# Optimization experiments

Hardware: AMD Instinct MI355X
Metric: run time of the kernel (lower is better)

Reference implementation:

```python
import jax, jax.numpy as jnp
import numpy as np

# Dims: batch, queries, graph nodes, text len, hidden, heads, layers, ffn
B, NQ, NN, T, D, H, LAYERS, FF = 16, 32, 128, 352, 768, 8, 6, 3072
L = NQ + NN + T          # 512 total sequence length
HD = D // H              # 96 head dim
NEG = -1e9               # additive mask value (HF uses dtype min; -1e9 is equivalent post-softmax)
LN_EPS = 1e-12           # BERT LayerNorm eps


def _ln(x, g, b):
    m = x.mean(-1, keepdims=True)
    v = ((x - m) ** 2).mean(-1, keepdims=True)
    return (x - m) * jax.lax.rsqrt(v + LN_EPS) * g + b


def setup_inputs() -> dict:
    key = jax.random.key(0)
    ks = iter(jax.random.split(key, 32))

    def nrm(shape, s=0.02):
        return jax.random.normal(next(ks), shape, jnp.float32) * s

    return {
        "graph_node_features": jax.random.normal(next(ks), (B, NN, D), jnp.float32),
        "text_embeds": jax.random.normal(next(ks), (B, T, D), jnp.float32),
        "text_atts": jnp.ones((B, T), jnp.int32),
        "graph_mask": jnp.ones((B, NN), jnp.int32),
        "query_tokens": nrm((1, NQ, D), 1.0),   # nn.Parameter(torch.randn(...))
        "gproj_w": nrm((D, D)), "gproj_b": jnp.zeros((D,)),
        "pos_emb": nrm((L, D)), "tok_emb": nrm((D,)),  # token_type row 0
        "emb_ln_g": jnp.ones((D,)), "emb_ln_b": jnp.zeros((D,)),
        "qkv_w": nrm((LAYERS, D, 3 * D)), "qkv_b": jnp.zeros((LAYERS, 3 * D)),
        "ao_w": nrm((LAYERS, D, D)), "ao_b": jnp.zeros((LAYERS, D)),
        "ln1_g": jnp.ones((LAYERS, D)), "ln1_b": jnp.zeros((LAYERS, D)),
        "ff1_w": nrm((LAYERS, D, FF)), "ff1_b": jnp.zeros((LAYERS, FF)),
        "ff2_w": nrm((LAYERS, FF, D)), "ff2_b": jnp.zeros((LAYERS, D)),
        "ln2_g": jnp.ones((LAYERS, D)), "ln2_b": jnp.zeros((LAYERS, D)),
    }


def _itg_bias(text_atts, graph_mask):
    # Build the custom ITG prefix-LM mask: bidirectional over [queries|graph],
    # causal over text, and queries/graph blocked from attending to text.
    keep = jnp.concatenate(
        [jnp.ones((B, NQ), jnp.int32), graph_mask, text_atts], axis=1)  # [B, L]
    ts = NQ + NN
    idx = jnp.arange(L)
    is_text = idx >= ts
    pair = (keep[:, :, None] * keep[:, None, :]).astype(bool)          # padding mask
    causal_ok = jnp.where(is_text[:, None] & is_text[None, :],
                          idx[:, None] >= idx[None, :], True)           # tril in text block
    block_ok = ~((~is_text)[:, None] & is_text[None, :])                # prefix cannot see text
    mask = pair & causal_ok & block_ok                                  # [B, L, L]
    return jnp.where(mask, 0.0, NEG)[:, None, :, :]                     # [B, 1, L, L]


def reference(graph_node_features, text_embeds, text_atts, graph_mask,
              query_tokens, gproj_w, gproj_b, pos_emb, tok_emb,
              emb_ln_g, emb_ln_b, qkv_w, qkv_b, ao_w, ao_b,
              ln1_g, ln1_b, ff1_w, ff1_b, ff2_w, ff2_b, ln2_g, ln2_b):
    gfeat = graph_node_features @ gproj_w + gproj_b
    qtok = jnp.broadcast_to(query_tokens, (B, NQ, D))
    x = jnp.concatenate([qtok, gfeat, text_embeds], axis=1)             # [B, L, D]
    bias = _itg_bias(text_atts, graph_mask)

    # BERT embeddings (inputs_embeds path): + position + token_type(0), LN (dropout off)
    x = _ln(x + pos_emb[None] + tok_emb, emb_ln_g, emb_ln_b)

    scale = 1.0 / np.sqrt(HD)
    for i in range(LAYERS):
        qkv = x @ qkv_w[i] + qkv_b[i]
        q, k, v = jnp.split(qkv, 3, axis=-1)
        q = q.reshape(B, L, H, HD)
        k = k.reshape(B, L, H, HD)
        v = v.reshape(B, L, H, HD)
        s = jnp.einsum('bqhd,bkhd->bhqk', q, k) * scale + bias
        p = jax.nn.softmax(s, axis=-1)
        ctx = jnp.einsum('bhqk,bkhd->bqhd', p, v).reshape(B, L, D)
        x = _ln(x + ctx @ ao_w[i] + ao_b[i], ln1_g[i], ln1_b[i])
        h = jax.nn.gelu(x @ ff1_w[i] + ff1_b[i], approximate=False)
        x = _ln(x + h @ ff2_w[i] + ff2_b[i], ln2_g[i], ln2_b[i])

    return x[:, NQ + NN:, :]   # text_feats [B, T, D]
```

## Files before the change

kernel.cpp:

```cpp
#include <hip/hip_runtime.h>
#include <math.h>

typedef __bf16 bf16;
typedef __bf16 bf16x8 __attribute__((ext_vector_type(8)));
typedef float f32x4 __attribute__((ext_vector_type(4)));

#define NQ   32
#define NN_  128
#define TT   352
#define DD   768
#define NH   8
#define HDIM 96
#define LSEQ 512
#define TSPLIT 160
#define FFD  3072
#define NLAYER 6
#define NBATCH 16

#define GLOAD(srcp, dstp)                                                     \
    __builtin_amdgcn_global_load_lds(                                         \
        (const __attribute__((address_space(1))) void*)(srcp),                \
        (__attribute__((address_space(3))) void*)(dstp), 16, 0, 0)

template <int ACT>
__global__ __launch_bounds__(256) void gemm_bt(
    const bf16* __restrict__ A, const bf16* __restrict__ Bt,
    bf16* __restrict__ C, const float* __restrict__ bias,
    int K, int lda, int ldb, int ldc, float alpha, int Nstore, size_t zstride)
{
    __shared__ __attribute__((aligned(16))) bf16 As[3 * 4096];
    __shared__ __attribute__((aligned(16))) bf16 Bs[3 * 4096];

    const int z = blockIdx.z;
    A  += (size_t)z * K;
    Bt += (size_t)z * K;
    C  += (size_t)z * zstride;

    const int n0 = blockIdx.x * 128, m0 = blockIdx.y * 128;
    const int t = threadIdx.x;
    const int w = t >> 6, l = t & 63;
    const int wm = w >> 1, wn = w & 1;
    const int lr = l & 15, quad = l >> 4;

    f32x4 acc[4][4] = {};

    const int f0 = w * 1024 + l * 8;
    const int ra0 = f0 >> 5, ca0 = f0 & 31;
    const int ra1 = (f0 + 512) >> 5, ca1 = (f0 + 512) & 31;
    const bf16* a0 = A  + (size_t)(m0 + ra0) * lda + ca0;
    const bf16* a1 = A  + (size_t)(m0 + ra1) * lda + ca1;
    const bf16* b0 = Bt + (size_t)(n0 + ra0) * ldb + ca0;
    const bf16* b1 = Bt + (size_t)(n0 + ra1) * ldb + ca1;

    const int nt = K >> 5;

    {
        bf16* pA = &As[w * 1024];
        bf16* pB = &Bs[w * 1024];
        GLOAD(a0, pA);        GLOAD(a1, pA + 512);
        GLOAD(b0, pB);        GLOAD(b1, pB + 512);
        pA += 4096;  pB += 4096;
        GLOAD(a0 + 32, pA);   GLOAD(a1 + 32, pA + 512);
        GLOAD(b0 + 32, pB);   GLOAD(b1 + 32, pB + 512);
    }

    int cb = 0, wb = 2;
    for (int T = 0; T < nt; ++T) {
        if (T == nt - 1) {
            asm volatile("s_waitcnt vmcnt(0)" ::: "memory");
        } else {
            asm volatile("s_waitcnt vmcnt(4)" ::: "memory");
        }
        __builtin_amdgcn_s_barrier();
        __builtin_amdgcn_sched_barrier(0);

        if (T + 2 < nt) {
            const int k0 = (T + 2) << 5;
            bf16* pA = &As[wb * 4096 + w * 1024];
            bf16* pB = &Bs[wb * 4096 + w * 1024];
            GLOAD(a0 + k0, pA);   GLOAD(a1 + k0, pA + 512);
            GLOAD(b0 + k0, pB);   GLOAD(b1 + k0, pB + 512);
        }

        const int cur = cb << 12;
        bf16x8 af[4], bf_[4];
#pragma unroll
        for (int i = 0; i < 4; ++i)
            af[i] = *(const bf16x8*)&As[cur + (wm * 64 + i * 16 + lr) * 32 + quad * 8];
#pragma unroll
        for (int j = 0; j < 4; ++j)
            bf_[j] = *(const bf16x8*)&Bs[cur + (wn * 64 + j * 16 + lr) * 32 + quad * 8];
#pragma unroll
        for (int i = 0; i < 4; ++i)
#pragma unroll
            for (int j = 0; j < 4; ++j)
                acc[i][j] = __builtin_amdgcn_mfma_f32_16x16x32_bf16(af[i], bf_[j], acc[i][j], 0, 0, 0);

        cb = (cb == 2) ? 0 : cb + 1;
        wb = (wb == 2) ? 0 : wb + 1;
    }

    const bool dob = (z == 0);
#pragma unroll
    for (int i = 0; i < 4; ++i) {
        const int grow = m0 + wm * 64 + i * 16 + quad * 4;
#pragma unroll
        for (int j = 0; j < 4; ++j) {
            const int gcol = n0 + wn * 64 + j * 16 + lr;
            if (gcol >= Nstore) continue;
            float bv = (bias && dob) ? bias[gcol] : 0.0f;
#pragma unroll
            for (int r = 0; r < 4; ++r) {
                float v = acc[i][j][r] * alpha + bv;
                if (ACT == 1) v = 0.5f * v * (1.0f + erff(v * 0.70710678118654752f));
                C[(size_t)(grow + r) * ldc + gcol] = (bf16)v;
            }
        }
    }
}

template <int ACT>
__global__ __launch_bounds__(512) void gemm_bt8(
    const bf16* __restrict__ A, const bf16* __restrict__ Bt,
    bf16* __restrict__ C, const float* __restrict__ bias,
    int K, int lda, int ldb, int ldc, float alpha, int Nstore)
{
    __shared__ __attribute__((aligned(16))) bf16 As[3 * 8192];
    __shared__ __attribute__((aligned(16))) bf16 Bs[3 * 4096];

    const int n0 = blockIdx.x * 128, m0 = blockIdx.y * 256;
    const int t = threadIdx.x;
    const int w = t >> 6, l = t & 63;
    const int wm = w >> 1, wn = w & 1;
    const int lr = l & 15, quad = l >> 4;

    f32x4 acc[4][4] = {};

    const int f0 = w * 512 + l * 8;
    const int ra0 = f0 >> 5,          ca0 = f0 & 31;
    const int ra1 = ((f0 + 4096) >> 5), ca1 = f0 & 31;
    const bf16* a0 = A  + (size_t)(m0 + ra0) * lda + ca0;
    const bf16* a1 = A  + (size_t)(m0 + ra1) * lda + ca1;
    const bf16* b0 = Bt + (size_t)(n0 + ra0) * ldb + ca0;

    const int nt = K >> 5;

    {
        bf16* pA = &As[w * 512];
        bf16* pB = &Bs[w * 512];
        GLOAD(a0, pA);        GLOAD(a1, pA + 4096);   GLOAD(b0, pB);
        pA += 8192;  pB += 4096;
        GLOAD(a0 + 32, pA);   GLOAD(a1 + 32, pA + 4096);  GLOAD(b0 + 32, pB);
    }

    int cb = 0, wb = 2;
    for (int T = 0; T < nt; ++T) {
        if (T == nt - 1) {
            asm volatile("s_waitcnt vmcnt(0)" ::: "memory");
        } else {
            asm volatile("s_waitcnt vmcnt(3)" ::: "memory");
        }
        __builtin_amdgcn_s_barrier();
        __builtin_amdgcn_sched_barrier(0);

        if (T + 2 < nt) {
            const int k0 = (T + 2) << 5;
            bf16* pA = &As[wb * 8192 + w * 512];
            bf16* pB = &Bs[wb * 4096 + w * 512];
            GLOAD(a0 + k0, pA);  GLOAD(a1 + k0, pA + 4096);  GLOAD(b0 + k0, pB);
        }

        const int curA = cb * 8192, curB = cb * 4096;
        bf16x8 af[4], bf_[4];
#pragma unroll
        for (int i = 0; i < 4; ++i)
            af[i] = *(const bf16x8*)&As[curA + (wm * 64 + i * 16 + lr) * 32 + quad * 8];
#pragma unroll
        for (int j = 0; j < 4; ++j)
            bf_[j] = *(const bf16x8*)&Bs[curB + (wn * 64 + j * 16 + lr) * 32 + quad * 8];

        __builtin_amdgcn_s_setprio(1);
#pragma unroll
        for (int i = 0; i < 4; ++i)
#pragma unroll
            for (int j = 0; j < 4; ++j)
                acc[i][j] = __builtin_amdgcn_mfma_f32_16x16x32_bf16(af[i], bf_[j], acc[i][j], 0, 0, 0);
        __builtin_amdgcn_s_setprio(0);

        cb = (cb == 2) ? 0 : cb + 1;
        wb = (wb == 2) ? 0 : wb + 1;
    }

#pragma unroll
    for (int i = 0; i < 4; ++i) {
        const int grow = m0 + wm * 64 + i * 16 + quad * 4;
#pragma unroll
        for (int j = 0; j < 4; ++j) {
            const int gcol = n0 + wn * 64 + j * 16 + lr;
            if (gcol >= Nstore) continue;
            float bv = bias ? bias[gcol] : 0.0f;
#pragma unroll
            for (int r = 0; r < 4; ++r) {
                float v = acc[i][j][r] * alpha + bv;
                if (ACT == 1) v = 0.5f * v * (1.0f + erff(v * 0.70710678118654752f));
                C[(size_t)(grow + r) * ldc + gcol] = (bf16)v;
            }
        }
    }
}

__global__ __launch_bounds__(256) void flash_attn(
    const bf16* __restrict__ qkv, bf16* __restrict__ ctx,
    const int* __restrict__ tatts, const int* __restrict__ gmask)
{
    __shared__ __attribute__((aligned(16))) bf16 Qs[64 * 104];
    __shared__ __attribute__((aligned(16))) bf16 Ks[64 * 104];
    __shared__ __attribute__((aligned(16))) bf16 Vs[96 * 72];
    __shared__ __attribute__((aligned(16))) bf16 Ps[64 * 72];
    __shared__ int keep[512];

    const int qt = blockIdx.x;
    const int bh = blockIdx.y;
    const int b = bh >> 3, h = bh & 7;
    const int q0 = qt * 64;
    const int t = threadIdx.x;
    const int w = t >> 6, l = t & 63;
    const int lr = l & 15, quad = l >> 4;
    const float scale = 0.10206207261596577f;

    const bf16* qbase = qkv + (size_t)b * 512 * 2304 + h * 96;
    const bf16* kbase = qbase + 768;
    const bf16* vbase = qbase + 1536;

    for (int j = t; j < 512; j += 256)
        keep[j] = (j < NQ) ? 1 : (j < TSPLIT ? gmask[b * NN_ + j - NQ]
                                             : tatts[b * TT + j - TSPLIT]);

#pragma unroll
    for (int c = 0; c < 3; ++c) {
        const int idx = t * 8 + c * 2048;
        const int r = idx / 96, d = idx % 96;
        *(bf16x8*)&Qs[r * 104 + d] =
            *(const bf16x8*)&qbase[(size_t)(q0 + r) * 2304 + d];
    }
    __syncthreads();

    int ki[4];
    int ig[4];
#pragma unroll
    for (int r = 0; r < 4; ++r) {
        ig[r] = q0 + w * 16 + quad * 4 + r;
        ki[r] = keep[ig[r]];
    }

    float m_run[4] = {-1e30f, -1e30f, -1e30f, -1e30f};
    float l_run[4] = {0.f, 0.f, 0.f, 0.f};
    f32x4 oc[6] = {};

    const int JMAX = (qt < 3) ? 128 : q0;
    for (int j0 = 0; j0 <= JMAX; j0 += 64) {
        __syncthreads();
#pragma unroll
        for (int c = 0; c < 3; ++c) {
            const int idx = t * 8 + c * 2048;
            const int r = idx / 96, d = idx % 96;
            *(bf16x8*)&Ks[r * 104 + d] =
                *(const bf16x8*)&kbase[(size_t)(j0 + r) * 2304 + d];
            bf16x8 vv = *(const bf16x8*)&vbase[(size_t)(j0 + r) * 2304 + d];
#pragma unroll
            for (int jj = 0; jj < 8; ++jj)
                Vs[(d + jj) * 72 + r] = vv[jj];
        }
        __syncthreads();

        bf16x8 aq[3];
#pragma unroll
        for (int ds = 0; ds < 3; ++ds)
            aq[ds] = *(const bf16x8*)&Qs[(w * 16 + lr) * 104 + ds * 32 + quad * 8];
        f32x4 sc[4];
#pragma unroll
        for (int cb = 0; cb < 4; ++cb) {
            f32x4 a = {};
#pragma unroll
            for (int ds = 0; ds < 3; ++ds) {
                bf16x8 bk = *(const bf16x8*)&Ks[(cb * 16 + lr) * 104 + ds * 32 + quad * 8];
                a = __builtin_amdgcn_mfma_f32_16x16x32_bf16(aq[ds], bk, a, 0, 0, 0);
            }
            sc[cb] = a;
        }

        float tm[4] = {-1e30f, -1e30f, -1e30f, -1e30f};
#pragma unroll
        for (int cb = 0; cb < 4; ++cb) {
            const int jg = j0 + cb * 16 + lr;
            const int kj = keep[jg];
#pragma unroll
            for (int r = 0; r < 4; ++r) {
                const int i = ig[r];
                bool ok = ki[r] && kj;
                if (i < TSPLIT && jg >= TSPLIT) ok = false;
                if (i >= TSPLIT && jg >= TSPLIT && i < jg) ok = false;
                float s = sc[cb][r] * scale + (ok ? 0.f : -1e9f);
                sc[cb][r] = s;
                tm[r] = fmaxf(tm[r], s);
            }
        }
#pragma unroll
        for (int off = 1; off < 16; off <<= 1)
#pragma unroll
            for (int r = 0; r < 4; ++r)
                tm[r] = fmaxf(tm[r], __shfl_xor(tm[r], off));

        float alpha_[4], ts[4] = {0.f, 0.f, 0.f, 0.f};
#pragma unroll
        for (int r = 0; r < 4; ++r) {
            const float mn = fmaxf(m_run[r], tm[r]);
            alpha_[r] = __expf(m_run[r] - mn);
            m_run[r] = mn;
            l_run[r] *= alpha_[r];
        }
#pragma unroll
        for (int db = 0; db < 6; ++db)
#pragma unroll
            for (int r = 0; r < 4; ++r)
                oc[db][r] *= alpha_[r];

#pragma unroll
        for (int cb = 0; cb < 4; ++cb)
#pragma unroll
            for (int r = 0; r < 4; ++r) {
                const float p = __expf(sc[cb][r] - m_run[r]);
                ts[r] += p;
                Ps[(w * 16 + quad * 4 + r) * 72 + cb * 16 + lr] = (bf16)p;
            }
#pragma unroll
        for (int off = 1; off < 16; off <<= 1)
#pragma unroll
            for (int r = 0; r < 4; ++r)
                ts[r] += __shfl_xor(ts[r], off);
#pragma unroll
        for (int r = 0; r < 4; ++r) l_run[r] += ts[r];

        __syncthreads();

#pragma unroll
        for (int l0 = 0; l0 < 64; l0 += 32) {
            bf16x8 ap = *(const bf16x8*)&Ps[(w * 16 + lr) * 72 + l0 + quad * 8];
#pragma unroll
            for (int db = 0; db < 6; ++db) {
                bf16x8 bv = *(const bf16x8*)&Vs[(db * 16 + lr) * 72 + l0 + quad * 8];
                oc[db] = __builtin_amdgcn_mfma_f32_16x16x32_bf16(ap, bv, oc[db], 0, 0, 0);
            }
        }
    }

#pragma unroll
    for (int r = 0; r < 4; ++r) {
        const float inv = 1.f / l_run[r];
        bf16* orow = ctx + ((size_t)b * 512 + ig[r]) * 768 + h * 96;
#pragma unroll
        for (int db = 0; db < 6; ++db)
            orow[db * 16 + lr] = (bf16)(oc[db][r] * inv);
    }
}

__global__ void transpose_w(const float* __restrict__ in, bf16* __restrict__ out,
                            int R, int C)
{
    __shared__ bf16 tile[32][33];
    const int c0 = blockIdx.x * 32, r0 = blockIdx.y * 32;
    const int tx = threadIdx.x & 31, ty = threadIdx.x >> 5;
    for (int i = ty; i < 32; i += 8)
        tile[i][tx] = (bf16)in[(size_t)(r0 + i) * C + c0 + tx];
    __syncthreads();
    for (int i = ty; i < 32; i += 8)
        out[(size_t)(c0 + i) * R + r0 + tx] = tile[tx][i];
}

__global__ void cvt_bf16(const float* __restrict__ in, bf16* __restrict__ out, int n)
{
    const int idx = blockIdx.x * 256 + threadIdx.x;
    if (idx < n) out[idx] = (bf16)in[idx];
}

__device__ __forceinline__ void block_reduce_2(float& a, float& b)
{
#pragma unroll
    for (int off = 32; off; off >>= 1) {
        a += __shfl_xor(a, off);
        b += __shfl_xor(b, off);
    }
    __shared__ float sa[4], sb[4];
    const int w = threadIdx.x >> 6;
    if ((threadIdx.x & 63) == 0) { sa[w] = a; sb[w] = b; }
    __syncthreads();
    a = sa[0] + sa[1] + sa[2] + sa[3];
    b = sb[0] + sb[1] + sb[2] + sb[3];
}

__global__ void embed_ln(const float* __restrict__ qtok, const bf16* __restrict__ gfeat,
                         const float* __restrict__ text, const float* __restrict__ pos,
                         const float* __restrict__ tok, const float* __restrict__ g,
                         const float* __restrict__ bb, bf16* __restrict__ x)
{
    const int row = blockIdx.x;
    const int l = row & 511, b = row >> 9;
    const int t = threadIdx.x;

    float vals[3], s = 0.f, sq = 0.f;
#pragma unroll
    for (int c = 0; c < 3; ++c) {
        const int d = t + c * 256;
        float base;
        if (l < NQ)           base = qtok[(size_t)l * DD + d];
        else if (l < TSPLIT)  base = (float)gfeat[((size_t)b * NN_ + (l - NQ)) * DD + d];
        else                  base = text[((size_t)b * TT + (l - TSPLIT)) * DD + d];
        float v = base + pos[(size_t)l * DD + d] + tok[d];
        vals[c] = v; s += v; sq += v * v;
    }
    block_reduce_2(s, sq);
    const float mean = s * (1.f / 768.f);
    const float var = sq * (1.f / 768.f) - mean * mean;
    const float rs = rsqrtf(var + 1e-12f);
    bf16* o = x + (size_t)row * DD;
#pragma unroll
    for (int c = 0; c < 3; ++c) {
        const int d = t + c * 256;
        o[d] = (bf16)((vals[c] - mean) * rs * g[d] + bb[d]);
    }
}

__global__ void ln_rows3(const bf16* __restrict__ X, const bf16* __restrict__ Y,
                         const bf16* __restrict__ Z, bf16* __restrict__ Out,
                         const float* __restrict__ g, const float* __restrict__ bb)
{
    const int row = blockIdx.x;
    const int t = threadIdx.x;
    const bf16* xr = X + (size_t)row * DD;
    const bf16* yr = Y + (size_t)row * DD;
    const bf16* zr = Z + (size_t)row * DD;
    float vals[3], s = 0.f, sq = 0.f;
#pragma unroll
    for (int c = 0; c < 3; ++c) {
        const int d = t + c * 256;
        float v = (float)xr[d] + (float)yr[d] + (float)zr[d];
        vals[c] = v; s += v; sq += v * v;
    }
    block_reduce_2(s, sq);
    const float mean = s * (1.f / 768.f);
    const float var = sq * (1.f / 768.f) - mean * mean;
    const float rs = rsqrtf(var + 1e-12f);
    bf16* o = Out + (size_t)row * DD;
#pragma unroll
    for (int c = 0; c < 3; ++c) {
        const int d = t + c * 256;
        o[d] = (bf16)((vals[c] - mean) * rs * g[d] + bb[d]);
    }
}

__global__ void copy_out(const bf16* __restrict__ x, float* __restrict__ out)
{
    const size_t idx = (size_t)blockIdx.x * 256 + threadIdx.x;
    const int d = idx % DD;
    const size_t row = idx / DD;
    const int t = row % TT;
    const int b = row / TT;
    out[idx] = (float)x[((size_t)b * LSEQ + TSPLIT + t) * DD + d];
}

static void launch_gemm(const bf16* A, const bf16* Bt, bf16* C, const float* bias,
                        int M, int K, int lda, int ldb, int ldc,
                        float alpha, int Nstore, int act, int ksplit, size_t zstride,
                        hipStream_t stream)
{
    dim3 grid((Nstore + 127) / 128, M / 128, ksplit);
    if (act)
        gemm_bt<1><<<grid, 256, 0, stream>>>(A, Bt, C, bias, K / ksplit, lda, ldb, ldc, alpha, Nstore, zstride);
    else
        gemm_bt<0><<<grid, 256, 0, stream>>>(A, Bt, C, bias, K / ksplit, lda, ldb, ldc, alpha, Nstore, zstride);
}

static void launch_gemm8(const bf16* A, const bf16* Bt, bf16* C, const float* bias,
                         int M, int K, int lda, int ldb, int ldc,
                         float alpha, int Nstore, int act, hipStream_t stream)
{
    dim3 grid((Nstore + 127) / 128, M / 256, 1);
    if (act)
        gemm_bt8<1><<<grid, 512, 0, stream>>>(A, Bt, C, bias, K, lda, ldb, ldc, alpha, Nstore);
    else
        gemm_bt8<0><<<grid, 512, 0, stream>>>(A, Bt, C, bias, K, lda, ldb, ldc, alpha, Nstore);
}

extern "C" void kernel_launch(void* const* d_in, const int* in_sizes, int n_in,
                              void* d_out, int out_size, void* d_ws, size_t ws_size,
                              hipStream_t stream)
{
    const float* gnf     = (const float*)d_in[0];
    const float* text    = (const float*)d_in[1];
    const int*   tatts   = (const int*)d_in[2];
    const int*   gmask   = (const int*)d_in[3];
    const float* qtok    = (const float*)d_in[4];
    const float* gproj_w = (const float*)d_in[5];
    const float* gproj_b = (const float*)d_in[6];
    const float* pos     = (const float*)d_in[7];
    const float* tok     = (const float*)d_in[8];
    const float* eg      = (const float*)d_in[9];
    const float* eb      = (const float*)d_in[10];
    const float* qkv_w   = (const float*)d_in[11];
    const float* qkv_b   = (const float*)d_in[12];
    const float* ao_w    = (const float*)d_in[13];
    const float* ao_b    = (const float*)d_in[14];
    const float* ln1g    = (const float*)d_in[15];
    const float* ln1b    = (const float*)d_in[16];
    const float* ff1_w   = (const float*)d_in[17];
    const float* ff1_b   = (const float*)d_in[18];
    const float* ff2_w   = (const float*)d_in[19];
    const float* ff2_b   = (const float*)d_in[20];
    const float* ln2g    = (const float*)d_in[21];
    const float* ln2b    = (const float*)d_in[22];
    float* out = (float*)d_out;

    bf16* ws   = (bf16*)d_ws;
    bf16* wt1  = ws;
    bf16* wt2  = wt1 + 2359296;
    bf16* x    = wt2 + 2359296;
    bf16* ctx  = x   + 6291456;
    bf16* t1   = ctx + 6291456;
    bf16* u    = t1  + 6291456;
    bf16* qkvb = u;
    bf16* hbuf = u;
    bf16* t2   = u   + 25165824;
    bf16* gfeat = t1;
    bf16* gnfb  = u;
    const size_t ZST = (size_t)(t2 - t1);

    dim3 blk(256);

    cvt_bf16<<<6144, blk, 0, stream>>>(gnf, gnfb, 1572864);
    transpose_w<<<dim3(24, 24), blk, 0, stream>>>(gproj_w, wt1, 768, 768);
    launch_gemm(gnfb, wt1, gfeat, gproj_b, 2048, 768, 768, 768, 768,
                1.f, 768, 0, 1, 0, stream);
    embed_ln<<<8192, blk, 0, stream>>>(qtok, gfeat, text, pos, tok, eg, eb, x);

    for (int i = 0; i < NLAYER; ++i) {
        transpose_w<<<dim3(72, 24), blk, 0, stream>>>(
            qkv_w + (size_t)i * 768 * 2304, wt1, 768, 2304);
        launch_gemm8(x, wt1, qkvb, qkv_b + i * 2304,
                     8192, 768, 768, 768, 2304, 1.f, 2304, 0, stream);
        flash_attn<<<dim3(8, 128), blk, 0, stream>>>(qkvb, ctx, tatts, gmask);
        transpose_w<<<dim3(24, 24), blk, 0, stream>>>(
            ao_w + (size_t)i * 589824, wt1, 768, 768);
        launch_gemm(ctx, wt1, t1, ao_b + i * 768,
                    8192, 768, 768, 768, 768, 1.f, 768, 0, 2, ZST, stream);
        ln_rows3<<<8192, blk, 0, stream>>>(x, t1, t2, x, ln1g + i * 768, ln1b + i * 768);

        transpose_w<<<dim3(96, 24), blk, 0, stream>>>(
            ff1_w + (size_t)i * 2359296, wt1, 768, 3072);
        transpose_w<<<dim3(24, 96), blk, 0, stream>>>(
            ff2_w + (size_t)i * 2359296, wt2, 3072, 768);
        launch_gemm8(x, wt1, hbuf, ff1_b + i * 3072,
                     8192, 768, 768, 768, 3072, 1.f, 3072, 1, stream);
        launch_gemm(hbuf, wt2, t1, ff2_b + i * 768,
                    8192, 3072, 3072, 3072, 768, 1.f, 768, 0, 2, ZST, stream);
        ln_rows3<<<8192, blk, 0, stream>>>(x, t1, t2, x, ln2g + i * 768, ln2b + i * 768);
    }

    copy_out<<<16896, blk, 0, stream>>>(x, out);

    (void)in_sizes; (void)n_in; (void)out_size; (void)ws_size;
}
```

Before: 2.141 ms.

## Load GEMM B operand directly into registers, dropping its LDS staging

Both GEMM kernels stop staging the B (weight) tile in shared memory. Each wave instead loads its MFMA B fragments straight from global memory into registers, double-buffered one k-step ahead, while A stays on the triple-buffered LDS path. The goals are to halve LDS footprint and traffic and to allow higher occupancy, hinted by the added launch-bounds minimum of 4 blocks. The cost is that B fragments are now loaded redundantly by the waves that share a column block, using uncoalesced 16-byte per-lane global reads. The main loop is also unrolled by two, which assumes nt is even, and the vmcnt wait counts are retuned for the mixed load types.

Measured after the change: 3.442 ms. 60.8% more time.

```diff
diff --git a/kernel.cpp b/kernel.cpp
--- a/kernel.cpp
+++ b/kernel.cpp
@@ -23,13 +23,12 @@
         (__attribute__((address_space(3))) void*)(dstp), 16, 0, 0)
 
 template <int ACT>
-__global__ __launch_bounds__(256) void gemm_bt(
+__global__ __launch_bounds__(256, 4) void gemm_bt(
     const bf16* __restrict__ A, const bf16* __restrict__ Bt,
     bf16* __restrict__ C, const float* __restrict__ bias,
     int K, int lda, int ldb, int ldc, float alpha, int Nstore, size_t zstride)
 {
     __shared__ __attribute__((aligned(16))) bf16 As[3 * 4096];
-    __shared__ __attribute__((aligned(16))) bf16 Bs[3 * 4096];
 
     const int z = blockIdx.z;
     A  += (size_t)z * K;
@@ -47,57 +46,73 @@
     const int f0 = w * 1024 + l * 8;
     const int ra0 = f0 >> 5, ca0 = f0 & 31;
     const int ra1 = (f0 + 512) >> 5, ca1 = (f0 + 512) & 31;
-    const bf16* a0 = A  + (size_t)(m0 + ra0) * lda + ca0;
-    const bf16* a1 = A  + (size_t)(m0 + ra1) * lda + ca1;
-    const bf16* b0 = Bt + (size_t)(n0 + ra0) * ldb + ca0;
-    const bf16* b1 = Bt + (size_t)(n0 + ra1) * ldb + ca1;
+    const bf16* a0 = A + (size_t)(m0 + ra0) * lda + ca0;
+    const bf16* a1 = A + (size_t)(m0 + ra1) * lda + ca1;
+
+    const bf16* bfr0 = Bt + (size_t)(n0 + wn * 64 +  0 + lr) * ldb + quad * 8;
+    const bf16* bfr1 = Bt + (size_t)(n0 + wn * 64 + 16 + lr) * ldb + quad * 8;
+    const bf16* bfr2 = Bt + (size_t)(n0 + wn * 64 + 32 + lr) * ldb + quad * 8;
+    const bf16* bfr3 = Bt + (size_t)(n0 + wn * 64 + 48 + lr) * ldb + quad * 8;
 
     const int nt = K >> 5;
+
+    bf16x8 be[4], bo[4];
 
     {
         bf16* pA = &As[w * 1024];
-        bf16* pB = &Bs[w * 1024];
-        GLOAD(a0, pA);        GLOAD(a1, pA + 512);
-        GLOAD(b0, pB);        GLOAD(b1, pB + 512);
-        pA += 4096;  pB += 4096;
-        GLOAD(a0 + 32, pA);   GLOAD(a1 + 32, pA + 512);
-        GLOAD(b0 + 32, pB);   GLOAD(b1 + 32, pB + 512);
+        GLOAD(a0, pA); GLOAD(a1, pA + 512);
+        be[0] = *(const bf16x8*)bfr0;
+        be[1] = *(const bf16x8*)bfr1;
+        be[2] = *(const bf16x8*)bfr2;
+        be[3] = *(const bf16x8*)bfr3;
+        pA += 4096;
+        GLOAD(a0 + 32, pA); GLOAD(a1 + 32, pA + 512);
     }
 
     int cb = 0, wb = 2;
-    for (int T = 0; T < nt; ++T) {
-        if (T == nt - 1) {
-            asm volatile("s_waitcnt vmcnt(0)" ::: "memory");
-        } else {
-            asm volatile("s_waitcnt vmcnt(4)" ::: "memory");
-        }
+
+    auto step = [&](int T, bf16x8 (&bcur)[4], bf16x8 (&bnext)[4]) {
+        if (T == nt - 1) { asm volatile("s_waitcnt vmcnt(4)" ::: "memory"); }
+        else             { asm volatile("s_waitcnt vmcnt(6)" ::: "memory"); }
         __builtin_amdgcn_s_barrier();
         __builtin_amdgcn_sched_barrier(0);
 
+        if (T + 1 < nt) {
+            const int ko = (T + 1) << 5;
+            bnext[0] = *(const bf16x8*)(bfr0 + ko);
+            bnext[1] = *(const bf16x8*)(bfr1 + ko);
+            bnext[2] = *(const bf16x8*)(bfr2 + ko);
+            bnext[3] = *(const bf16x8*)(bfr3 + ko);
+        }
         if (T + 2 < nt) {
-            const int k0 = (T + 2) << 5;
+            const int ko = (T + 2) << 5;
             bf16* pA = &As[wb * 4096 + w * 1024];
-            bf16* pB = &Bs[wb * 4096 + w * 1024];
-            GLOAD(a0 + k0, pA);   GLOAD(a1 + k0, pA + 512);
-            GLOAD(b0 + k0, pB);   GLOAD(b1 + k0, pB + 512);
+            GLOAD(a0 + ko, pA); GLOAD(a1 + ko, pA + 512);
         }
 
         const int cur = cb << 12;
-        bf16x8 af[4], bf_[4];
+        bf16x8 af[4];
 #pragma unroll
         for (int i = 0; i < 4; ++i)
             af[i] = *(const bf16x8*)&As[cur + (wm * 64 + i * 16 + lr) * 32 + quad * 8];
-#pragma unroll
-        for (int j = 0; j < 4; ++j)
-            bf_[j] = *(const bf16x8*)&Bs[cur + (wn * 64 + j * 16 + lr) * 32 + quad * 8];
-#pragma unroll
-        for (int i = 0; i < 4; ++i)
-#pragma unroll
-            for (int j = 0; j < 4; ++j)
-                acc[i][j] = __builtin_amdgcn_mfma_f32_16x16x32_bf16(af[i], bf_[j], acc[i][j], 0, 0, 0);
+
+        __builtin_amdgcn_s_setprio(1);
+#pragma unroll
+        for (int i = 0; i < 4; ++i) {
+            acc[i][0] = __builtin_amdgcn_mfma_f32_16x16x32_bf16(af[i], bcur[0], acc[i][0], 0, 0, 0);
+            acc[i][1] = __builtin_amdgcn_mfma_f32_16x16x32_bf16(af[i], bcur[1], acc[i][1], 0, 0, 0);
+            acc[i][2] = __builtin_amdgcn_mfma_f32_16x16x32_bf16(af[i], bcur[2], acc[i][2], 0, 0, 0);
+            acc[i][3] = __builtin_amdgcn_mfma_f32_16x16x32_bf16(af[i], bcur[3], acc[i][3], 0, 0, 0);
+        }
+        __builtin_amdgcn_s_setprio(0);
 
         cb = (cb == 2) ? 0 : cb + 1;
         wb = (wb == 2) ? 0 : wb + 1;
+    };
+
+    for (int T = 0; T < nt; T += 2) {
+        step(T, be, bo);
+        step(T + 1, bo, be);
     }
 
     const bool dob = (z == 0);
@@ -120,13 +135,12 @@
 }
 
 template <int ACT>
-__global__ __launch_bounds__(512) void gemm_bt8(
+__global__ __launch_bounds__(512, 4) void gemm_bt8(
     const bf16* __restrict__ A, const bf16* __restrict__ Bt,
     bf16* __restrict__ C, const float* __restrict__ bias,
     int K, int lda, int ldb, int ldc, float alpha, int Nstore)
 {
     __shared__ __attribute__((aligned(16))) bf16 As[3 * 8192];
-    __shared__ __attribute__((aligned(16))) bf16 Bs[3 * 4096];
 
     const int n0 = blockIdx.x * 128, m0 = blockIdx.y * 256;
     const int t = threadIdx.x;
@@ -137,58 +151,75 @@
     f32x4 acc[4][4] = {};
 
     const int f0 = w * 512 + l * 8;
-    const int ra0 = f0 >> 5,          ca0 = f0 & 31;
+    const int ra0 = f0 >> 5,            ca0 = f0 & 31;
     const int ra1 = ((f0 + 4096) >> 5), ca1 = f0 & 31;
-    const bf16* a0 = A  + (size_t)(m0 + ra0) * lda + ca0;
-    const bf16* a1 = A  + (size_t)(m0 + ra1) * lda + ca1;
-    const bf16* b0 = Bt + (size_t)(n0 + ra0) * ldb + ca0;
+    const bf16* a0 = A + (size_t)(m0 + ra0) * lda + ca0;
+    const bf16* a1 = A + (size_t)(m0 + ra1) * lda + ca1;
+
+    const bf16* bfr0 = Bt + (size_t)(n0 + wn * 64 +  0 + lr) * ldb + quad * 8;
+    const bf16* bfr1 = Bt + (size_t)(n0 + wn * 64 + 16 + lr) * ldb + quad * 8;
+    const bf16* bfr2 = Bt + (size_t)(n0 + wn * 64 + 32 + lr) * ldb + quad * 8;
+    const bf16* bfr3 = Bt + (size_t)(n0 + wn * 64 + 48 + lr) * ldb + quad * 8;
 
     const int nt = K >> 5;
+
+    bf16x8 be[4], bo[4];
 
     {
         bf16* pA = &As[w * 512];
-        bf16* pB = &Bs[w * 512];
-        GLOAD(a0, pA);        GLOAD(a1, pA + 4096);   GLOAD(b0, pB);
-        pA += 8192;  pB += 4096;
-        GLOAD(a0 + 32, pA);   GLOAD(a1 + 32, pA + 4096);  GLOAD(b0 + 32, pB);
+        GLOAD(a0, pA); GLOAD(a1, pA + 4096);
+        be[0] = *(const bf16x8*)bfr0;
+        be[1] = *(const bf16x8*)bfr1;
+        be[2] = *(const bf16x8*)bfr2;
+        be[3] = *(const bf16x8*)bfr3;
+        pA += 8192;
+        GLOAD(a0 + 32, pA); GLOAD(a1 + 32, pA + 4096);
     }
 
     int cb = 0, wb = 2;
-    for (int T = 0; T < nt; ++T) {
-        if (T == nt - 1) {
-            asm volatile("s_waitcnt vmcnt(0)" ::: "memory");
-        } else {
-            asm volatile("s_waitcnt vmcnt(3)" ::: "memory");
-        }
+
+    auto step = [&](int T, bf16x8 (&bcur)[4], bf16x8 (&bnext)[4]) {
+        if (T == nt - 1) { asm volatile("s_waitcnt vmcnt(4)" ::: "memory"); }
+        else             { asm volatile("s_waitcnt vmcnt(6)" ::: "memory"); }
         __builtin_amdgcn_s_barrier();
         __builtin_amdgcn_sched_barrier(0);
 
+        if (T + 1 < nt) {
+            const int ko = (T + 1) << 5;
+            bnext[0] = *(const bf16x8*)(bfr0 + ko);
+            bnext[1] = *(const bf16x8*)(bfr1 + ko);
+            bnext[2] = *(const bf16x8*)(bfr2 + ko);
+            bnext[3] = *(const bf16x8*)(bfr3 + ko);
+        }
         if (T + 2 < nt) {
-            const int k0 = (T + 2) << 5;
+            const int ko = (T + 2) << 5;
             bf16* pA = &As[wb * 8192 + w * 512];
-            bf16* pB = &Bs[wb * 4096 + w * 512];
-            GLOAD(a0 + k0, pA);  GLOAD(a1 + k0, pA + 4096);  GLOAD(b0 + k0, pB);
-        }
-
-        const int curA = cb * 8192, curB = cb * 4096;
-        bf16x8 af[4], bf_[4];
+            GLOAD(a0 + ko, pA); GLOAD(a1 + ko, pA + 4096);
+        }
+
+        const int curA = cb * 8192;
+        bf16x8 af[4];
 #pragma unroll
         for (int i = 0; i < 4; ++i)
             af[i] = *(const bf16x8*)&As[curA + (wm * 64 + i * 16 + lr) * 32 + quad * 8];
-#pragma unroll
-        for (int j = 0; j < 4; ++j)
-            bf_[j] = *(const bf16x8*)&Bs[curB + (wn * 64 + j * 16 + lr) * 32 + quad * 8];
 
         __builtin_amdgcn_s_setprio(1);
 #pragma unroll
-        for (int i = 0; i < 4; ++i)
-#pragma unroll
-            for (int j = 0; j < 4; ++j)
-                acc[i][j] = __builtin_amdgcn_mfma_f32_16x16x32_bf16(af[i], bf_[j], acc[i][j], 0, 0, 0);
+        for (int i = 0; i < 4; ++i) {
+            acc[i][0] = __builtin_amdgcn_mfma_f32_16x16x32_bf16(af[i], bcur[0], acc[i][0], 0, 0, 0);
+            acc[i][1] = __builtin_amdgcn_mfma_f32_16x16x32_bf16(af[i], bcur[1], acc[i][1], 0, 0, 0);
+            acc[i][2] = __builtin_amdgcn_mfma_f32_16x16x32_bf16(af[i], bcur[2], acc[i][2], 0, 0, 0);
+            acc[i][3] = __builtin_amdgcn_mfma_f32_16x16x32_bf16(af[i], bcur[3], acc[i][3], 0, 0, 0);
+        }
         __builtin_amdgcn_s_setprio(0);
 
         cb = (cb == 2) ? 0 : cb + 1;
         wb = (wb == 2) ? 0 : wb + 1;
+    };
+
+    for (int T = 0; T < nt; T += 2) {
+        step(T, be, bo);
+        step(T + 1, bo, be);
     }
 
 #pragma unroll
```
